# Optimization experiments

Hardware: AMD Instinct MI355X
Metric: run time of the kernel (lower is better)

Reference implementation:

```python
import jax, jax.numpy as jnp
import numpy as np

N_USERS = 20000
N_ITEMS = 20000
H0, H1, H2 = 256, 512, 256  # hidden = [256, 512, 256]
B = 4096
LN_EPS = 1e-5


def _ln(x, g, b):
    m = jnp.mean(x, axis=-1, keepdims=True)
    v = jnp.mean(jnp.square(x - m), axis=-1, keepdims=True)
    return (x - m) * jax.lax.rsqrt(v + LN_EPS) * g + b


def setup_inputs() -> dict:
    key = jax.random.key(0)
    ks = jax.random.split(key, 12)
    s = 0.02
    inp = {
        "user_idx": jax.random.randint(ks[0], (B,), 0, N_USERS),
        "item_idx": jax.random.randint(ks[1], (B,), 0, N_ITEMS),
        # (n_users+1, n_items+1) binary interaction matrix, stored as bool
        "interactions": jax.random.bernoulli(ks[2], 0.05, (N_USERS + 1, N_ITEMS + 1)),
        # proj_u / proj_i (bias=False), torch Linear layout (out, in)
        "Wu": jax.random.normal(ks[3], (H0, N_ITEMS), jnp.float32) * s,
        "Wi": jax.random.normal(ks[4], (H0, N_USERS), jnp.float32) * s,
        # rep_u: Linear(H0,H1)+LN+ReLU, Linear(H1,H2)+LN+ReLU (dropout=eval identity)
        "W1": jax.random.normal(ks[5], (H1, H0), jnp.float32) * s,
        "b1": jnp.zeros((H1,), jnp.float32),
        "g1": jnp.ones((H1,), jnp.float32),
        "be1": jnp.zeros((H1,), jnp.float32),
        "W2": jax.random.normal(ks[6], (H2, H1), jnp.float32) * s,
        "b2": jnp.zeros((H2,), jnp.float32),
        "g2": jnp.ones((H2,), jnp.float32),
        "be2": jnp.zeros((H2,), jnp.float32),
        # logit layer
        "Wl": jax.random.normal(ks[7], (1, H2), jnp.float32) * s,
        "bl": jnp.zeros((1,), jnp.float32),
    }
    return inp


def reference(user_idx, item_idx, interactions, Wu, Wi, W1, b1, g1, be1,
              W2, b2, g2, be2, Wl, bl):
    b_arange = jnp.arange(user_idx.shape[0])

    # --- user history embedding: gather row, zero target item, project, MLP ---
    u_slice = interactions[user_idx, :-1].astype(jnp.float32)      # (B, n_items)
    u_slice = u_slice.at[b_arange, item_idx].set(0.0)
    u = u_slice @ Wu.T                                             # (B, H0)
    u = jax.nn.relu(_ln(u @ W1.T + b1, g1, be1))                   # (B, H1)
    user_rep = jax.nn.relu(_ln(u @ W2.T + b2, g2, be2))            # (B, H2)

    # --- item history embedding: gather column, zero target user, project ---
    i_slice = interactions.T[item_idx][:, :-1].astype(jnp.float32)  # (B, n_users)
    i_slice = i_slice.at[b_arange, user_idx].set(0.0)
    item_rep = i_slice @ Wi.T                                      # (B, H0); rep_i is an empty Sequential in source

    pred_vector = user_rep * item_rep                              # (B, H2) == (B, H0)
    logit = (pred_vector @ Wl.T + bl).squeeze(-1)                  # (B,)
    return logit
```

## Files before the change

kernel.cpp:

```cpp
#include <hip/hip_runtime.h>

#define N_USERS 20000
#define N_ITEMS 20000
#define NI1     20001
#define HB      4096
#define H0      256
#define H1      512
#define H2      256
#define PKW     632
#define PKB     (PKW*4)
#define NWF     12501251

typedef unsigned short u16;
typedef unsigned char  u8;
typedef unsigned int   u32;
typedef unsigned long long u64;

typedef __attribute__((ext_vector_type(8))) __bf16 bf16x8;
typedef __attribute__((ext_vector_type(4))) float  f32x4;

__device__ __forceinline__ u16 f2bf(float f) {
  u32 u = __float_as_uint(f);
  u32 r = (u + 0x7FFFu + ((u >> 16) & 1u)) >> 16;
  return (u16)r;
}

__global__ __launch_bounds__(256) void k_detect(const u8* __restrict__ inter,
                                                int* __restrict__ flag) {
  __shared__ u32 cnt[4];
  if (threadIdx.x < 4) cnt[threadIdx.x] = 0;
  __syncthreads();
  u32 loc0 = 0, loc1 = 0, loc2 = 0, loc3 = 0;
  for (int i = threadIdx.x; i < 16384; i += 256) {
    u32 w = ((const u32*)inter)[i];
    loc0 += (w & 0x000000FFu) ? 1u : 0u;
    loc1 += (w & 0x0000FF00u) ? 1u : 0u;
    loc2 += (w & 0x00FF0000u) ? 1u : 0u;
    loc3 += (w & 0xFF000000u) ? 1u : 0u;
  }
  atomicAdd(&cnt[0], loc0); atomicAdd(&cnt[1], loc1);
  atomicAdd(&cnt[2], loc2); atomicAdd(&cnt[3], loc3);
  __syncthreads();
  if (threadIdx.x == 0) {
    int lay;
    if (cnt[1] != 0)      lay = 0;
    else if (cnt[0] != 0) lay = 1;
    else                  lay = 2;
    *flag = lay;
  }
}

template <int LAY>
__global__ __launch_bounds__(256) void k_packF(const u8* __restrict__ inter,
                                               u32* __restrict__ pkF,
                                               const int* __restrict__ flag) {
  if (*flag != LAY) return;
  int stride = gridDim.x * 256;
  for (int wi = blockIdx.x * 256 + threadIdx.x; wi < NWF; wi += stride) {
    u32 m = 0;
    if (wi < NWF - 1) {
      if (LAY == 0) {
        const uint4* p = (const uint4*)(inter + (size_t)wi * 32);
        uint4 a = p[0], b = p[1];
        u32 ww[8] = {a.x, a.y, a.z, a.w, b.x, b.y, b.z, b.w};
        #pragma unroll
        for (int q = 0; q < 8; ++q)
          #pragma unroll
          for (int j = 0; j < 4; ++j)
            m |= (((ww[q] >> (8 * j)) & 0xFFu) ? 1u : 0u) << (q * 4 + j);
      } else {
        const uint4* p = (const uint4*)(inter + (size_t)wi * 128);
        #pragma unroll
        for (int q = 0; q < 8; ++q) {
          uint4 v = p[q];
          m |= (v.x ? 1u : 0u) << (q * 4)     | (v.y ? 1u : 0u) << (q * 4 + 1)
             | (v.z ? 1u : 0u) << (q * 4 + 2) | (v.w ? 1u : 0u) << (q * 4 + 3);
        }
      }
    } else {
      const size_t TE = (size_t)NI1 * NI1;
      for (int j = 0; j < 32; ++j) {
        size_t e = (size_t)wi * 32 + j;
        if (e < TE) {
          bool p = (LAY == 0) ? (inter[e] != 0) : (((const u32*)inter)[e] != 0u);
          m |= (p ? 1u : 0u) << j;
        }
      }
    }
    pkF[wi] = m;
  }
}

__global__ __launch_bounds__(256) void k_realign(const u32* __restrict__ pkF,
                                                 u32* __restrict__ pk) {
  int r = blockIdx.x;
  int base = 625 * r + (r >> 5);
  int s = r & 31;
  for (int w = threadIdx.x; w < PKW; w += 256) {
    u32 val = 0;
    if (w < 625) {
      u32 lo = pkF[base + w];
      u32 hi = pkF[base + w + 1];
      val = s ? ((lo >> s) | (hi << (32 - s))) : lo;
    }
    pk[(size_t)r * PKW + w] = val;
  }
}

#define HDSTEP(J, M)                                      \
  _Pragma("unroll")                                       \
  for (int k = 0; k < 32; ++k) if (!(k & J)) {            \
    u32 tt = (a[k] ^ (a[k | J] >> J)) & M;                \
    a[k] ^= tt; a[k | J] ^= tt << J;                      \
  }

__global__ __launch_bounds__(256) void k_bitT(const u32* __restrict__ pk,
                                              u32* __restrict__ pkT) {
  __shared__ u32 in_l[512][17];
  __shared__ u32 out_l[32][16][17];
  int t = threadIdx.x;
  int vt = blockIdx.x % 40, wt = blockIdx.x / 40;
  int v0 = vt * 16, wc0 = wt * 16;
  int lw = t & 15, lr = t >> 4;
  for (int ch = 0; ch < 32; ++ch) {
    int rloc = ch * 16 + lr;
    int R = v0 * 32 + rloc;
    int W = wc0 + lw;
    u32 val = 0;
    if (R < N_USERS && W < PKW) val = pk[(size_t)R * PKW + W];
    in_l[rloc][lw] = val;
  }
  __syncthreads();
  u32 a[32];
  #pragma unroll
  for (int j = 0; j < 32; ++j) a[j] = in_l[lr * 32 + j][lw];
  HDSTEP(16, 0x0000FFFFu)
  HDSTEP(8,  0x00FF00FFu)
  HDSTEP(4,  0x0F0F0F0Fu)
  HDSTEP(2,  0x33333333u)
  HDSTEP(1,  0x55555555u)
  #pragma unroll
  for (int i = 0; i < 32; ++i) out_l[i][lw][lr] = __brev(a[31 - i]);
  __syncthreads();
  for (int ch = 0; ch < 32; ++ch) {
    int rloc = ch * 16 + lr;
    int C = wc0 * 32 + rloc;
    int V = v0 + lw;
    if (C < N_ITEMS && V < PKW)
      pkT[(size_t)C * PKW + V] = out_l[rloc & 31][rloc >> 5][lw];
  }
}

__global__ __launch_bounds__(256) void k_convert(const float* __restrict__ in,
                                                 u16* __restrict__ out, int n4) {
  int idx = blockIdx.x * 256 + threadIdx.x;
  int stride = gridDim.x * 256;
  for (int i = idx; i < n4; i += stride) {
    float4 v = ((const float4*)in)[i];
    u64 p = (u64)f2bf(v.x) | ((u64)f2bf(v.y) << 16) |
            ((u64)f2bf(v.z) << 32) | ((u64)f2bf(v.w) << 48);
    ((u64*)out)[i] = p;
  }
}

__global__ __launch_bounds__(256) void k_transpose(const float* __restrict__ in,
                                                   float* __restrict__ out,
                                                   int R, int C) {
  __shared__ float tile[32][33];
  int nbx = C >> 5;
  int bx = blockIdx.x % nbx, by = blockIdx.x / nbx;
  int c0 = bx * 32, r0 = by * 32;
  int lx = threadIdx.x & 31, ly = threadIdx.x >> 5;
  #pragma unroll
  for (int j = 0; j < 4; ++j)
    tile[ly + 8*j][lx] = in[(size_t)(r0 + ly + 8*j) * C + c0 + lx];
  __syncthreads();
  #pragma unroll
  for (int j = 0; j < 4; ++j)
    out[(size_t)(c0 + ly + 8*j) * R + r0 + lx] = tile[lx][ly + 8*j];
}

__global__ __launch_bounds__(1024) void k_sort(const int* __restrict__ item_idx,
                                               int* __restrict__ perm) {
  __shared__ u32 cnt[N_ITEMS];
  __shared__ u32 tsum[1024];
  int t = threadIdx.x;
  for (int i = t; i < N_ITEMS; i += 1024) cnt[i] = 0;
  __syncthreads();
  for (int b = t; b < HB; b += 1024) atomicAdd(&cnt[item_idx[b]], 1u);
  __syncthreads();
  u32 s = 0;
  int base = t * 20;
  for (int j = 0; j < 20; ++j) { int i = base + j; if (i < N_ITEMS) s += cnt[i]; }
  tsum[t] = s;
  __syncthreads();
  for (int off = 1; off < 1024; off <<= 1) {
    u32 v = (t >= off) ? tsum[t - off] : 0u;
    __syncthreads();
    tsum[t] += v;
    __syncthreads();
  }
  u32 run = tsum[t] - s;
  for (int j = 0; j < 20; ++j) {
    int i = base + j;
    if (i < N_ITEMS) { u32 c = cnt[i]; cnt[i] = run; run += c; }
  }
  __syncthreads();
  for (int b = t; b < HB; b += 1024) {
    int v = item_idx[b];
    u32 pos = atomicAdd(&cnt[v], 1u);
    perm[pos] = b;
  }
}

__global__ __launch_bounds__(256) void k_gemm(
    const u32* __restrict__ pk, const u32* __restrict__ pkT,
    const int* __restrict__ user_idx, const int* __restrict__ item_idx,
    const int* __restrict__ perm,
    const u16* __restrict__ Wub, const u16* __restrict__ Wib,
    float* __restrict__ u0, float* __restrict__ ir) {
  __shared__ __attribute__((aligned(16))) u16 Bls[32 * 128];
  __shared__ __attribute__((aligned(16))) uint2 lut8[16];
  __shared__ u32 pbase[128];
  __shared__ int prow[128];

  int bid = blockIdx.x;
  int mode_item = bid >> 8;
  int lid = bid & 255;
  int M0 = (lid >> 3) * 128;
  int N0 = (lid & 7) * 32;
  int tid = threadIdx.x;
  const u16* Wb = mode_item ? Wib : Wub;
  const u8* Pk = (const u8*)(mode_item ? pkT : pk);
  float* Cout = mode_item ? ir : u0;

  if (tid < 16) {
    u32 v = tid;
    lut8[tid].x = ((v & 1u) ? 0x3F80u : 0u) | ((v & 2u) ? 0x3F800000u : 0u);
    lut8[tid].y = ((v & 4u) ? 0x3F80u : 0u) | ((v & 8u) ? 0x3F800000u : 0u);
  }
  if (tid < 128) {
    int s = M0 + tid;
    if (mode_item) { int p = perm[s]; prow[tid] = p; pbase[tid] = (u32)item_idx[p] * PKB; }
    else           { prow[tid] = s;   pbase[tid] = (u32)user_idx[s] * PKB; }
  }
  __syncthreads();

  f32x4 acc[2][2];
  #pragma unroll
  for (int a = 0; a < 2; ++a)
    #pragma unroll
    for (int b = 0; b < 2; ++b)
      #pragma unroll
      for (int j = 0; j < 4; ++j) acc[a][b][j] = 0.f;

  int lane = tid & 63, wave = tid >> 6;
  int WM = wave * 32;
  int lrow = lane & 15;
  int lk8 = lane >> 4;
  int sh = lk8 * 8;

  u32 pb0 = pbase[WM + lrow];
  u32 pb1 = pbase[WM + 16 + lrow];

  for (int k0 = 0; k0 < 20096; k0 += 128) {
    #pragma unroll
    for (int i = 0; i < 2; ++i) {
      int id = tid + 256 * i;
      int n = id >> 4, c8 = id & 15;
      int k = k0 + c8 * 8;
      uint4 v = make_uint4(0u, 0u, 0u, 0u);
      if (k < N_ITEMS) v = *(const uint4*)&Wb[(size_t)(N0 + n) * N_ITEMS + k];
      int off = n * 128 + ((c8 * 8) ^ ((n & 7) << 3));
      *(uint4*)&Bls[off] = v;
    }
    uint4 qa0 = *(const uint4*)(Pk + pb0 + (k0 >> 3));
    uint4 qa1 = *(const uint4*)(Pk + pb1 + (k0 >> 3));
    u32 qw0[4] = {qa0.x, qa0.y, qa0.z, qa0.w};
    u32 qw1[4] = {qa1.x, qa1.y, qa1.z, qa1.w};
    __syncthreads();
    #pragma unroll
    for (int kki = 0; kki < 4; ++kki) {
      u32 b0 = (qw0[kki] >> sh) & 0xFFu;
      u32 b1 = (qw1[kki] >> sh) & 0xFFu;
      union { u32 w[4]; bf16x8 v; } a0, a1;
      uint2 l0 = lut8[b0 & 15u], h0 = lut8[b0 >> 4];
      uint2 l1 = lut8[b1 & 15u], h1 = lut8[b1 >> 4];
      a0.w[0] = l0.x; a0.w[1] = l0.y; a0.w[2] = h0.x; a0.w[3] = h0.y;
      a1.w[0] = l1.x; a1.w[1] = l1.y; a1.w[2] = h1.x; a1.w[3] = h1.y;
      bf16x8 bfr[2];
      #pragma unroll
      for (int fn = 0; fn < 2; ++fn) {
        int n = fn * 16 + lrow;
        bfr[fn] = *(const bf16x8*)&Bls[n * 128 + ((kki * 32 + sh) ^ ((n & 7) << 3))];
      }
      acc[0][0] = __builtin_amdgcn_mfma_f32_16x16x32_bf16(a0.v, bfr[0], acc[0][0], 0, 0, 0);
      acc[0][1] = __builtin_amdgcn_mfma_f32_16x16x32_bf16(a0.v, bfr[1], acc[0][1], 0, 0, 0);
      acc[1][0] = __builtin_amdgcn_mfma_f32_16x16x32_bf16(a1.v, bfr[0], acc[1][0], 0, 0, 0);
      acc[1][1] = __builtin_amdgcn_mfma_f32_16x16x32_bf16(a1.v, bfr[1], acc[1][1], 0, 0, 0);
    }
    __syncthreads();
  }

  int crow0 = (lane >> 4) * 4;
  int ccol = lane & 15;
  #pragma unroll
  for (int fm = 0; fm < 2; ++fm)
    #pragma unroll
    for (int fn = 0; fn < 2; ++fn) {
      f32x4 v = acc[fm][fn];
      int col = N0 + fn * 16 + ccol;
      #pragma unroll
      for (int j = 0; j < 4; ++j) {
        int rl = WM + fm * 16 + crow0 + j;
        Cout[(size_t)prow[rl] * H0 + col] = v[j];
      }
    }
}

__global__ __launch_bounds__(256) void k_mlp(
    const u32* __restrict__ pk,
    const int* __restrict__ user_idx, const int* __restrict__ item_idx,
    const float* __restrict__ Wu, const float* __restrict__ Wi,
    const float* __restrict__ u0, const float* __restrict__ ir,
    const float* __restrict__ W1T, const float* __restrict__ b1,
    const float* __restrict__ g1, const float* __restrict__ be1,
    const float* __restrict__ W2T, const float* __restrict__ b2,
    const float* __restrict__ g2, const float* __restrict__ be2,
    const float* __restrict__ Wl, const float* __restrict__ bl,
    float* __restrict__ out) {
  __shared__ __attribute__((aligned(16))) float xl[16][H0];
  __shared__ __attribute__((aligned(16))) float h1l[16][H1];
  __shared__ int flagL[16], uL[16], iL[16];

  int tid = threadIdx.x, lane = tid & 63, wave = tid >> 6;
  int b0 = blockIdx.x * 16;

  if (tid < 16) {
    int b = b0 + tid;
    int uu = user_idx[b], ii = item_idx[b];
    uL[tid] = uu; iL[tid] = ii;
    u8 byte = ((const u8*)pk)[(size_t)uu * PKB + (ii >> 3)];
    flagL[tid] = (byte >> (ii & 7)) & 1;
  }
  __syncthreads();

  for (int idx = tid; idx < 16 * H0; idx += 256) {
    int rr = idx >> 8, h = idx & 255;
    float x = u0[(size_t)(b0 + rr) * H0 + h];
    if (flagL[rr]) x -= Wu[(size_t)h * N_ITEMS + iL[rr]];
    xl[rr][h] = x;
  }
  __syncthreads();

  float a0[16], a1[16];
  #pragma unroll
  for (int rr = 0; rr < 16; ++rr) { a0[rr] = 0.f; a1[rr] = 0.f; }
  for (int k4 = 0; k4 < H0 / 4; ++k4) {
    int k = k4 * 4;
    float w0a = W1T[(size_t)(k+0)*H1 + tid], w0b = W1T[(size_t)(k+0)*H1 + tid + 256];
    float w1a = W1T[(size_t)(k+1)*H1 + tid], w1b = W1T[(size_t)(k+1)*H1 + tid + 256];
    float w2a = W1T[(size_t)(k+2)*H1 + tid], w2b = W1T[(size_t)(k+2)*H1 + tid + 256];
    float w3a = W1T[(size_t)(k+3)*H1 + tid], w3b = W1T[(size_t)(k+3)*H1 + tid + 256];
    #pragma unroll
    for (int rr = 0; rr < 16; ++rr) {
      float4 x = *(const float4*)&xl[rr][k];
      a0[rr] += x.x * w0a + x.y * w1a + x.z * w2a + x.w * w3a;
      a1[rr] += x.x * w0b + x.y * w1b + x.z * w2b + x.w * w3b;
    }
  }
  #pragma unroll
  for (int rr = 0; rr < 16; ++rr) {
    h1l[rr][tid]       = a0[rr] + b1[tid];
    h1l[rr][tid + 256] = a1[rr] + b1[tid + 256];
  }
  __syncthreads();

  for (int rr = wave; rr < 16; rr += 4) {
    float s = 0.f;
    #pragma unroll
    for (int j = 0; j < 8; ++j) s += h1l[rr][lane + 64 * j];
    #pragma unroll
    for (int off = 32; off; off >>= 1) s += __shfl_xor(s, off);
    float m = s * (1.f / H1);
    float v = 0.f;
    #pragma unroll
    for (int j = 0; j < 8; ++j) { float d = h1l[rr][lane + 64*j] - m; v += d * d; }
    #pragma unroll
    for (int off = 32; off; off >>= 1) v += __shfl_xor(v, off);
    float inv = rsqrtf(v * (1.f / H1) + 1e-5f);
    #pragma unroll
    for (int j = 0; j < 8; ++j) {
      int o = lane + 64 * j;
      float y = (h1l[rr][o] - m) * inv * g1[o] + be1[o];
      h1l[rr][o] = fmaxf(y, 0.f);
    }
  }
  __syncthreads();

  float a2[16];
  #pragma unroll
  for (int rr = 0; rr < 16; ++rr) a2[rr] = 0.f;
  for (int k4 = 0; k4 < H1 / 4; ++k4) {
    int k = k4 * 4;
    float w0 = W2T[(size_t)(k+0)*H2 + tid];
    float w1 = W2T[(size_t)(k+1)*H2 + tid];
    float w2 = W2T[(size_t)(k+2)*H2 + tid];
    float w3 = W2T[(size_t)(k+3)*H2 + tid];
    #pragma unroll
    for (int rr = 0; rr < 16; ++rr) {
      float4 x = *(const float4*)&h1l[rr][k];
      a2[rr] += x.x * w0 + x.y * w1 + x.z * w2 + x.w * w3;
    }
  }
  __syncthreads();
  #pragma unroll
  for (int rr = 0; rr < 16; ++rr) xl[rr][tid] = a2[rr] + b2[tid];
  __syncthreads();

  for (int rr = wave; rr < 16; rr += 4) {
    float s = 0.f;
    #pragma unroll
    for (int j = 0; j < 4; ++j) s += xl[rr][lane + 64 * j];
    #pragma unroll
    for (int off = 32; off; off >>= 1) s += __shfl_xor(s, off);
    float m = s * (1.f / H2);
    float v = 0.f;
    #pragma unroll
    for (int j = 0; j < 4; ++j) { float d = xl[rr][lane + 64*j] - m; v += d * d; }
    #pragma unroll
    for (int off = 32; off; off >>= 1) v += __shfl_xor(v, off);
    float inv = rsqrtf(v * (1.f / H2) + 1e-5f);
    #pragma unroll
    for (int j = 0; j < 4; ++j) {
      int o = lane + 64 * j;
      float y = (xl[rr][o] - m) * inv * g2[o] + be2[o];
      xl[rr][o] = fmaxf(y, 0.f);
    }
  }
  __syncthreads();

  for (int rr = wave; rr < 16; rr += 4) {
    int b = b0 + rr;
    int flg = flagL[rr], uu = uL[rr];
    float s = 0.f;
    #pragma unroll
    for (int j = 0; j < 4; ++j) {
      int h = lane + 64 * j;
      float irv = ir[(size_t)b * H0 + h];
      if (flg) irv -= Wi[(size_t)h * N_USERS + uu];
      s += xl[rr][h] * irv * Wl[h];
    }
    #pragma unroll
    for (int off = 32; off; off >>= 1) s += __shfl_xor(s, off);
    if (lane == 0) out[b] = s + bl[0];
  }
}

extern "C" void kernel_launch(void* const* d_in, const int* in_sizes, int n_in,
                              void* d_out, int out_size, void* d_ws, size_t ws_size,
                              hipStream_t stream) {
  const int*   user_idx = (const int*)d_in[0];
  const int*   item_idx = (const int*)d_in[1];
  const u8*    inter    = (const u8*)d_in[2];
  const float* Wu  = (const float*)d_in[3];
  const float* Wi  = (const float*)d_in[4];
  const float* W1  = (const float*)d_in[5];
  const float* b1  = (const float*)d_in[6];
  const float* g1  = (const float*)d_in[7];
  const float* be1 = (const float*)d_in[8];
  const float* W2  = (const float*)d_in[9];
  const float* b2  = (const float*)d_in[10];
  const float* g2  = (const float*)d_in[11];
  const float* be2 = (const float*)d_in[12];
  const float* Wl  = (const float*)d_in[13];
  const float* bl  = (const float*)d_in[14];
  float* out = (float*)d_out;

  char* ws = (char*)d_ws;
  size_t off = 0;
  auto alloc = [&](size_t bytes) {
    size_t o = off;
    off = (off + bytes + 255) & ~(size_t)255;
    return o;
  };
  int*   flag = (int*)  (ws + alloc(4));
  u32*   pkF  = (u32*)  (ws + alloc((size_t)(NWF + 64) * 4));
  u32*   pk   = (u32*)  (ws + alloc((size_t)N_USERS * PKB));
  u32*   pkT  = (u32*)  (ws + alloc((size_t)N_ITEMS * PKB));
  u16*   Wub  = (u16*)  (ws + alloc((size_t)H0 * N_ITEMS * 2));
  u16*   Wib  = (u16*)  (ws + alloc((size_t)H0 * N_USERS * 2));
  float* W1T  = (float*)(ws + alloc((size_t)H0 * H1 * 4));
  float* W2T  = (float*)(ws + alloc((size_t)H1 * H2 * 4));
  float* u0   = (float*)(ws + alloc((size_t)HB * H0 * 4));
  float* ir   = (float*)(ws + alloc((size_t)HB * H0 * 4));
  int*   perm = (int*)  (ws + alloc((size_t)HB * 4));

  k_detect<<<1, 256, 0, stream>>>(inter, flag);
  k_packF<0><<<3072, 256, 0, stream>>>(inter, pkF, flag);
  k_packF<1><<<3072, 256, 0, stream>>>(inter, pkF, flag);
  k_packF<2><<<3072, 256, 0, stream>>>(inter, pkF, flag);
  k_realign<<<N_USERS, 256, 0, stream>>>(pkF, pk);
  k_bitT<<<1600, 256, 0, stream>>>(pk, pkT);
  k_convert<<<512, 256, 0, stream>>>(Wu, Wub, (H0 * N_ITEMS) / 4);
  k_convert<<<512, 256, 0, stream>>>(Wi, Wib, (H0 * N_USERS) / 4);
  k_transpose<<<(H1 / 32) * (H0 / 32), 256, 0, stream>>>(W1, W1T, H1, H0);
  k_transpose<<<(H2 / 32) * (H1 / 32), 256, 0, stream>>>(W2, W2T, H2, H1);
  k_sort<<<1, 1024, 0, stream>>>(item_idx, perm);
  k_gemm<<<512, 256, 0, stream>>>(pk, pkT, user_idx, item_idx, perm, Wub, Wib, u0, ir);
  k_mlp<<<256, 256, 0, stream>>>(pk, user_idx, item_idx, Wu, Wi, u0, ir,
                                 W1T, b1, g1, be1, W2T, b2, g2, be2, Wl, bl, out);
}
```

Measured before the change: 727.6 us.

## Coalesce bit-packing reads via LDS nibble staging and merge small prep kernels

The bit-packing kernel now has each wave read contiguous 16-byte chunks with lane-strided addressing, build 4-bit nibbles in shared memory, and then assemble 32-bit words, replacing per-thread strided 32/128-byte reads. The three layout-specialised launches are collapsed into one kernel that branches on the runtime flag. The two bf16 conversion launches and the two weight-transpose launches are each merged into a single launch to cut launch overhead. The cost is extra LDS traffic and two block-wide barriers per group in the packing kernel.

```diff
diff --git a/kernel.cpp b/kernel.cpp
--- a/kernel.cpp
+++ b/kernel.cpp
@@ -50,44 +50,59 @@
   }
 }
 
-template <int LAY>
 __global__ __launch_bounds__(256) void k_packF(const u8* __restrict__ inter,
                                                u32* __restrict__ pkF,
                                                const int* __restrict__ flag) {
-  if (*flag != LAY) return;
-  int stride = gridDim.x * 256;
-  for (int wi = blockIdx.x * 256 + threadIdx.x; wi < NWF; wi += stride) {
-    u32 m = 0;
-    if (wi < NWF - 1) {
-      if (LAY == 0) {
-        const uint4* p = (const uint4*)(inter + (size_t)wi * 32);
-        uint4 a = p[0], b = p[1];
-        u32 ww[8] = {a.x, a.y, a.z, a.w, b.x, b.y, b.z, b.w};
+  int lay = *flag;
+  __shared__ u32 nibs[4][8][64];
+  const size_t TE = (size_t)NI1 * NI1;
+  const int NG = (int)((TE + 8191) / 8192);
+  int wave = threadIdx.x >> 6, lane = threadIdx.x & 63;
+  const u32* base32 = (const u32*)inter;
+  for (int g = blockIdx.x; g < NG; g += gridDim.x) {
+    size_t E0 = (size_t)g * 8192 + (size_t)wave * 2048;
+    bool full = ((size_t)(g + 1) * 8192) <= TE;
+    if (lay != 0) {
+      if (full) {
         #pragma unroll
-        for (int q = 0; q < 8; ++q)
+        for (int t = 0; t < 8; ++t) {
+          size_t e = E0 + (size_t)t * 256 + lane * 4;
+          uint4 v = *(const uint4*)(base32 + e);
+          nibs[wave][t][lane] = (v.x ? 1u : 0u) | (v.y ? 2u : 0u) |
+                                (v.z ? 4u : 0u) | (v.w ? 8u : 0u);
+        }
+      } else {
+        #pragma unroll
+        for (int t = 0; t < 8; ++t) {
+          size_t e = E0 + (size_t)t * 256 + lane * 4;
+          u32 n = 0;
           #pragma unroll
-          for (int j = 0; j < 4; ++j)
-            m |= (((ww[q] >> (8 * j)) & 0xFFu) ? 1u : 0u) << (q * 4 + j);
-      } else {
-        const uint4* p = (const uint4*)(inter + (size_t)wi * 128);
-        #pragma unroll
-        for (int q = 0; q < 8; ++q) {
-          uint4 v = p[q];
-          m |= (v.x ? 1u : 0u) << (q * 4)     | (v.y ? 1u : 0u) << (q * 4 + 1)
-             | (v.z ? 1u : 0u) << (q * 4 + 2) | (v.w ? 1u : 0u) << (q * 4 + 3);
+          for (int c = 0; c < 4; ++c)
+            if (e + c < TE && base32[e + c]) n |= 1u << c;
+          nibs[wave][t][lane] = n;
         }
       }
     } else {
-      const size_t TE = (size_t)NI1 * NI1;
-      for (int j = 0; j < 32; ++j) {
-        size_t e = (size_t)wi * 32 + j;
-        if (e < TE) {
-          bool p = (LAY == 0) ? (inter[e] != 0) : (((const u32*)inter)[e] != 0u);
-          m |= (p ? 1u : 0u) << j;
-        }
+      #pragma unroll
+      for (int t = 0; t < 8; ++t) {
+        size_t e = E0 + (size_t)t * 256 + lane * 4;
+        u32 n = 0;
+        #pragma unroll
+        for (int c = 0; c < 4; ++c)
+          if (e + c < TE && inter[e + c]) n |= 1u << c;
+        nibs[wave][t][lane] = n;
       }
     }
-    pkF[wi] = m;
+    __syncthreads();
+    {
+      int t = lane >> 3, j = lane & 7;
+      u32 wrd = 0;
+      #pragma unroll
+      for (int k = 0; k < 8; ++k) wrd |= nibs[wave][t][8 * j + k] << (4 * k);
+      size_t wg = (size_t)g * 256 + wave * 64 + lane;
+      if (wg < NWF) pkF[wg] = wrd;
+    }
+    __syncthreads();
   }
 }
 
@@ -151,24 +166,34 @@
   }
 }
 
-__global__ __launch_bounds__(256) void k_convert(const float* __restrict__ in,
-                                                 u16* __restrict__ out, int n4) {
-  int idx = blockIdx.x * 256 + threadIdx.x;
+__global__ __launch_bounds__(256) void k_convert2(const float* __restrict__ Wu,
+                                                  const float* __restrict__ Wi,
+                                                  u16* __restrict__ Wub,
+                                                  u16* __restrict__ Wib) {
+  const int n4 = H0 * N_ITEMS / 4;
   int stride = gridDim.x * 256;
-  for (int i = idx; i < n4; i += stride) {
-    float4 v = ((const float4*)in)[i];
+  for (int i = blockIdx.x * 256 + threadIdx.x; i < 2 * n4; i += stride) {
+    const float* in = (i < n4) ? Wu : Wi;
+    u16* out = (i < n4) ? Wub : Wib;
+    int idx = (i < n4) ? i : i - n4;
+    float4 v = ((const float4*)in)[idx];
     u64 p = (u64)f2bf(v.x) | ((u64)f2bf(v.y) << 16) |
             ((u64)f2bf(v.z) << 32) | ((u64)f2bf(v.w) << 48);
-    ((u64*)out)[i] = p;
-  }
-}
-
-__global__ __launch_bounds__(256) void k_transpose(const float* __restrict__ in,
-                                                   float* __restrict__ out,
-                                                   int R, int C) {
+    ((u64*)out)[idx] = p;
+  }
+}
+
+__global__ __launch_bounds__(256) void k_transpose2(const float* __restrict__ W1,
+                                                    float* __restrict__ W1T,
+                                                    const float* __restrict__ W2,
+                                                    float* __restrict__ W2T) {
   __shared__ float tile[32][33];
+  int bid = blockIdx.x;
+  const float* in; float* out; int R, C, b;
+  if (bid < 128) { in = W1; out = W1T; R = H1; C = H0; b = bid; }
+  else           { in = W2; out = W2T; R = H2; C = H1; b = bid - 128; }
   int nbx = C >> 5;
-  int bx = blockIdx.x % nbx, by = blockIdx.x / nbx;
+  int bx = b % nbx, by = b / nbx;
   int c0 = bx * 32, r0 = by * 32;
   int lx = threadIdx.x & 31, ly = threadIdx.x >> 5;
   #pragma unroll
@@ -497,15 +522,11 @@
   int*   perm = (int*)  (ws + alloc((size_t)HB * 4));
 
   k_detect<<<1, 256, 0, stream>>>(inter, flag);
-  k_packF<0><<<3072, 256, 0, stream>>>(inter, pkF, flag);
-  k_packF<1><<<3072, 256, 0, stream>>>(inter, pkF, flag);
-  k_packF<2><<<3072, 256, 0, stream>>>(inter, pkF, flag);
+  k_packF<<<3072, 256, 0, stream>>>(inter, pkF, flag);
   k_realign<<<N_USERS, 256, 0, stream>>>(pkF, pk);
   k_bitT<<<1600, 256, 0, stream>>>(pk, pkT);
-  k_convert<<<512, 256, 0, stream>>>(Wu, Wub, (H0 * N_ITEMS) / 4);
-  k_convert<<<512, 256, 0, stream>>>(Wi, Wib, (H0 * N_USERS) / 4);
-  k_transpose<<<(H1 / 32) * (H0 / 32), 256, 0, stream>>>(W1, W1T, H1, H0);
-  k_transpose<<<(H2 / 32) * (H1 / 32), 256, 0, stream>>>(W2, W2T, H2, H1);
+  k_convert2<<<1024, 256, 0, stream>>>(Wu, Wi, Wub, Wib);
+  k_transpose2<<<256, 256, 0, stream>>>(W1, W1T, W2, W2T);
   k_sort<<<1, 1024, 0, stream>>>(item_idx, perm);
   k_gemm<<<512, 256, 0, stream>>>(pk, pkT, user_idx, item_idx, perm, Wub, Wib, u0, ir);
   k_mlp<<<256, 256, 0, stream>>>(pk, user_idx, item_idx, Wu, Wi, u0, ir,
```

After: 719.1 us. No clear change (-1.2%).
